# Kernel optimization log

Measured on AMD Instinct MI355X. Metric: run time of the kernel, lower is better.

Reference implementation:

```python
import jax, jax.numpy as jnp
import numpy as np

N, Z, E, M0, M1, D = 16384, 100, 400, 4000, 2000, 4


def setup_inputs() -> dict:
    key = jax.random.key(0)
    k = jax.random.split(key, 7)
    return {
        "theta": jax.random.normal(k[0], (N, Z), jnp.float32),
        "alpha0": jax.random.normal(k[1], (M0, E), jnp.float32),
        "alpha1": jax.random.normal(k[2], (M1, E), jnp.float32),
        "beta": jax.random.normal(k[3], (Z, E), jnp.float32),
        "bias0": jax.random.normal(k[4], (D, M0), jnp.float32),
        "bias1": jax.random.normal(k[5], (D, M1), jnp.float32),
        "domain_idx": jax.random.randint(k[6], (N,), 0, D, dtype=jnp.int32),
    }


def _recon_mod(theta, alpha, beta, bias, domain_idx):
    # Topic_mod = (alpha @ beta.T).T == beta @ alpha.T : (Z, M)
    topic = beta @ alpha.T
    # per-domain GEMM + indexed bias-add + log_softmax + scatter-back
    # == single GEMM with per-row gathered bias (all domains present)
    logits = theta @ topic + bias[domain_idx]  # (N, M)
    return jax.nn.log_softmax(logits, axis=-1)


def reference(theta, alpha0, alpha1, beta, bias0, bias1, domain_idx):
    r0 = _recon_mod(theta, alpha0, beta, bias0, domain_idx)
    r1 = _recon_mod(theta, alpha1, beta, bias1, domain_idx)
    return (r0, r1)
```

## Files before the change

### kernel.cpp

```cpp
#include <hip/hip_runtime.h>
#include <hip/hip_bf16.h>

#define PN 16384
#define PZ 100
#define PE 400
#define PM0 4000
#define PM1 2000
#define KP 128
#define SEG1ROW 4096
#define MROWS 6144

typedef __attribute__((ext_vector_type(8))) _Float16 half8v;
typedef __attribute__((ext_vector_type(4))) float floatx4;
typedef __attribute__((ext_vector_type(4))) unsigned int uint4v;

__global__ __launch_bounds__(256) void fill_kernel(uint4v* __restrict__ p, int n16)
{
    int i = blockIdx.x * 256 + threadIdx.x;
    if (i < n16) p[i] = (uint4v){0u, 0u, 0u, 0u};
}

__global__ __launch_bounds__(256) void topic_kernel(
    const float* __restrict__ alpha0, const float* __restrict__ alpha1,
    const float* __restrict__ beta, _Float16* __restrict__ b2t)
{
    const int seg = (blockIdx.x >= 64);
    const int tile = seg ? (blockIdx.x - 64) : blockIdx.x;
    const float* alpha = seg ? alpha1 : alpha0;
    const int M = seg ? PM1 : PM0;
    const int rowbase = seg ? SEG1ROW : 0;

    __shared__ float sA[64][201];
    const int tid = threadIdx.x;
    const int ml = tid & 63;
    const int zt = tid >> 6;
    const int m0 = tile * 64;
    const int z0 = blockIdx.y * 20 + zt * 5;

    float acc[5] = {0.f, 0.f, 0.f, 0.f, 0.f};

    for (int ec = 0; ec < 2; ++ec) {
        #pragma unroll
        for (int l = 0; l < 50; ++l) {
            int idx = tid + l * 256;
            int mr = idx / 200;
            int e  = idx - mr * 200;
            int m  = m0 + mr;
            sA[mr][e] = (m < M) ? alpha[(size_t)m * PE + ec * 200 + e] : 0.f;
        }
        __syncthreads();
        const float* bz = beta + (size_t)z0 * PE + ec * 200;
        #pragma unroll 4
        for (int e = 0; e < 200; ++e) {
            float a = sA[ml][e];
            #pragma unroll
            for (int zi = 0; zi < 5; ++zi)
                acc[zi] = fmaf(bz[zi * PE + e], a, acc[zi]);
        }
        __syncthreads();
    }
    int m = m0 + ml;
    if (m < M) {
        #pragma unroll
        for (int zi = 0; zi < 5; ++zi)
            b2t[(size_t)(rowbase + m) * KP + (z0 + zi)] = (_Float16)acc[zi];
    }
}

__global__ __launch_bounds__(512, 4) void fused_kernel(
    const float* __restrict__ theta,
    const _Float16* __restrict__ B2T,
    const float* __restrict__ bias0, const float* __restrict__ bias1,
    const int* __restrict__ dom,
    float* __restrict__ out0, float* __restrict__ out1)
{
    __shared__ __align__(1024) char sA[8192];
    __shared__ float smx[8][32];
    __shared__ float sms[8][32];
    __shared__ float slse[32];

    const int tid = threadIdx.x;
    const int w   = tid >> 6;
    const int ll  = tid & 63;
    const int g   = ll >> 4;
    const int c   = ll & 15;
    const int n0  = blockIdx.x * 32;

    {
        int row  = tid >> 4;
        int slot = tid & 15;
        const float* tr = theta + (size_t)(n0 + row) * PZ + slot * 8;
        half8v h;
        if (slot < 12) {
            float4 lo = *(const float4*)tr;
            float4 hi = *(const float4*)(tr + 4);
            h[0] = (_Float16)lo.x; h[1] = (_Float16)lo.y;
            h[2] = (_Float16)lo.z; h[3] = (_Float16)lo.w;
            h[4] = (_Float16)hi.x; h[5] = (_Float16)hi.y;
            h[6] = (_Float16)hi.z; h[7] = (_Float16)hi.w;
        } else if (slot == 12) {
            float4 lo = *(const float4*)tr;
            h[0] = (_Float16)lo.x; h[1] = (_Float16)lo.y;
            h[2] = (_Float16)lo.z; h[3] = (_Float16)lo.w;
            h[4] = (_Float16)0.f; h[5] = (_Float16)0.f;
            h[6] = (_Float16)0.f; h[7] = (_Float16)0.f;
        } else {
            h = (half8v)(_Float16)0.f;
        }
        *(half8v*)(sA + row * 256 + ((slot ^ (row & 7)) * 16)) = h;
    }
    __syncthreads();

    half8v aF[2][4];
    #pragma unroll
    for (int mi = 0; mi < 2; ++mi) {
        int row = mi * 16 + c;
        #pragma unroll
        for (int kb = 0; kb < 4; ++kb) {
            int slot = (kb * 4 + g) ^ (row & 7);
            aF[mi][kb] = *(const half8v*)(sA + row * 256 + slot * 16);
        }
    }

    int drow[2][4];
    #pragma unroll
    for (int mi = 0; mi < 2; ++mi)
        #pragma unroll
        for (int i = 0; i < 4; ++i)
            drow[mi][i] = dom[n0 + mi * 16 + 4 * g + i];

    for (int seg = 0; seg < 2; ++seg) {
        const int Mse = seg ? PM1 : PM0;
        const int NT  = seg ? 16 : 32;
        const _Float16* Bseg = B2T + (size_t)(seg ? SEG1ROW : 0) * KP;
        const float* bias = seg ? bias1 : bias0;
        float* out = seg ? out1 : out0;

        const _Float16* bcol = Bseg + (size_t)(w * 16 + c) * KP;
        const int mbase = w * 16 + c;

        float mx_[2][4], sm_[2][4];
        #pragma unroll
        for (int mi = 0; mi < 2; ++mi)
            #pragma unroll
            for (int i = 0; i < 4; ++i) { mx_[mi][i] = -3.0e38f; sm_[mi][i] = 0.f; }

        for (int t = 0; t < NT; ++t) {
            const int m  = t * 128 + mbase;
            const _Float16* bp = bcol + (size_t)t * 128 * KP;
            half8v bF[4];
            #pragma unroll
            for (int kb = 0; kb < 4; ++kb)
                bF[kb] = *(const half8v*)(bp + kb * 32 + g * 8);

            const bool mv = (m < Mse);
            const int mc = mv ? m : (Mse - 1);
            float bv0 = bias[mc];
            float bv1 = bias[(size_t)Mse + mc];
            float bv2 = bias[2 * (size_t)Mse + mc];
            float bv3 = bias[3 * (size_t)Mse + mc];

            floatx4 acc[2];
            acc[0] = (floatx4){0.f, 0.f, 0.f, 0.f};
            acc[1] = (floatx4){0.f, 0.f, 0.f, 0.f};
            #pragma unroll
            for (int mi = 0; mi < 2; ++mi)
                #pragma unroll
                for (int kb = 0; kb < 4; ++kb)
                    acc[mi] = __builtin_amdgcn_mfma_f32_16x16x32_f16(
                        aF[mi][kb], bF[kb], acc[mi], 0, 0, 0);

            float vv[2][4];
            float gm = -3.0e38f;
            #pragma unroll
            for (int mi = 0; mi < 2; ++mi) {
                #pragma unroll
                for (int i = 0; i < 4; ++i) {
                    int d = drow[mi][i];
                    float bv = (d < 2) ? (d == 0 ? bv0 : bv1) : (d == 2 ? bv2 : bv3);
                    float v = mv ? (acc[mi][i] + bv) : -1.0e30f;
                    vv[mi][i] = v;
                    gm = fmaxf(gm, v - mx_[mi][i]);
                }
            }
            if (gm <= 8.0f) {
                #pragma unroll
                for (int mi = 0; mi < 2; ++mi)
                    #pragma unroll
                    for (int i = 0; i < 4; ++i)
                        sm_[mi][i] += __expf(vv[mi][i] - mx_[mi][i]);
            } else {
                #pragma unroll
                for (int mi = 0; mi < 2; ++mi) {
                    #pragma unroll
                    for (int i = 0; i < 4; ++i) {
                        float v  = vv[mi][i];
                        float nm = fmaxf(mx_[mi][i], v);
                        sm_[mi][i] = sm_[mi][i] * __expf(mx_[mi][i] - nm)
                                   + __expf(v - nm);
                        mx_[mi][i] = nm;
                    }
                }
            }
        }

        #pragma unroll
        for (int mi = 0; mi < 2; ++mi) {
            #pragma unroll
            for (int i = 0; i < 4; ++i) {
                float m_ = mx_[mi][i], s_ = sm_[mi][i];
                #pragma unroll
                for (int msk = 1; msk < 16; msk <<= 1) {
                    float mo = __shfl_xor(m_, msk);
                    float so = __shfl_xor(s_, msk);
                    float nm = fmaxf(m_, mo);
                    s_ = s_ * __expf(m_ - nm) + so * __expf(mo - nm);
                    m_ = nm;
                }
                if (c == 0) {
                    int row = mi * 16 + 4 * g + i;
                    smx[w][row] = m_;
                    sms[w][row] = s_;
                }
            }
        }
        __syncthreads();
        if (tid < 32) {
            float m_ = smx[0][tid], s_ = sms[0][tid];
            #pragma unroll
            for (int wv = 1; wv < 8; ++wv) {
                float mo = smx[wv][tid];
                float so = sms[wv][tid];
                float nm = fmaxf(m_, mo);
                s_ = s_ * __expf(m_ - nm) + so * __expf(mo - nm);
                m_ = nm;
            }
            slse[tid] = m_ + __logf(s_);
        }
        __syncthreads();
        float lse_[2][4];
        #pragma unroll
        for (int mi = 0; mi < 2; ++mi)
            #pragma unroll
            for (int i = 0; i < 4; ++i)
                lse_[mi][i] = slse[mi * 16 + 4 * g + i];
        __syncthreads();

        for (int t = 0; t < NT; ++t) {
            const int m  = t * 128 + mbase;
            const _Float16* bp = bcol + (size_t)t * 128 * KP;
            half8v bF[4];
            #pragma unroll
            for (int kb = 0; kb < 4; ++kb)
                bF[kb] = *(const half8v*)(bp + kb * 32 + g * 8);

            const bool mv = (m < Mse);
            const int mc = mv ? m : (Mse - 1);
            float bv0 = bias[mc];
            float bv1 = bias[(size_t)Mse + mc];
            float bv2 = bias[2 * (size_t)Mse + mc];
            float bv3 = bias[3 * (size_t)Mse + mc];

            floatx4 acc[2];
            acc[0] = (floatx4){0.f, 0.f, 0.f, 0.f};
            acc[1] = (floatx4){0.f, 0.f, 0.f, 0.f};
            #pragma unroll
            for (int mi = 0; mi < 2; ++mi)
                #pragma unroll
                for (int kb = 0; kb < 4; ++kb)
                    acc[mi] = __builtin_amdgcn_mfma_f32_16x16x32_f16(
                        aF[mi][kb], bF[kb], acc[mi], 0, 0, 0);

            if (mv) {
                #pragma unroll
                for (int mi = 0; mi < 2; ++mi) {
                    #pragma unroll
                    for (int i = 0; i < 4; ++i) {
                        int row = mi * 16 + 4 * g + i;
                        int d = drow[mi][i];
                        float bv = (d < 2) ? (d == 0 ? bv0 : bv1)
                                           : (d == 2 ? bv2 : bv3);
                        float o = acc[mi][i] + bv - lse_[mi][i];
                        __builtin_nontemporal_store(
                            o, &out[(size_t)(n0 + row) * Mse + m]);
                    }
                }
            }
        }
    }
}

extern "C" void kernel_launch(void* const* d_in, const int* in_sizes, int n_in,
                              void* d_out, int out_size, void* d_ws, size_t ws_size,
                              hipStream_t stream) {
    const float* theta  = (const float*)d_in[0];
    const float* alpha0 = (const float*)d_in[1];
    const float* alpha1 = (const float*)d_in[2];
    const float* beta   = (const float*)d_in[3];
    const float* bias0  = (const float*)d_in[4];
    const float* bias1  = (const float*)d_in[5];
    const int*   dom    = (const int*)d_in[6];

    float* out0 = (float*)d_out;
    float* out1 = out0 + (size_t)PN * PM0;

    _Float16* B2T = (_Float16*)d_ws;

    {
        int n16 = MROWS * KP * 2 / 16;
        fill_kernel<<<(n16 + 255) / 256, 256, 0, stream>>>((uint4v*)B2T, n16);
    }

    topic_kernel<<<dim3(96, 5), 256, 0, stream>>>(alpha0, alpha1, beta, B2T);

    fused_kernel<<<PN / 32, 512, 0, stream>>>(
        theta, B2T, bias0, bias1, dom, out0, out1);
}
```

Before: 315.1 us.

## Fold per-domain bias into GEMM via one-hot K columns; prefetch B tiles

Each theta row gets a one-hot domain vector in the padded K columns (100..103), and the topic kernel writes the matching bias rows into B2T, so the MFMA now produces logits with the bias already added. This removes the four scalar bias gathers and the per-element domain select from both passes of the fused kernel. The topic kernel now computes all 100 topics per block, stages its output in LDS and zeroes the padding itself, which drops the separate fill kernel launch. The fused kernel double-buffers B fragment loads across tiles. The risk is that bias is now rounded to fp16 inside the GEMM, which changes precision, and the topic kernel runs on far fewer blocks with more registers each.

```diff
diff --git a/kernel.cpp b/kernel.cpp
--- a/kernel.cpp
+++ b/kernel.cpp
@@ -14,30 +14,33 @@
 typedef __attribute__((ext_vector_type(4))) float floatx4;
 typedef __attribute__((ext_vector_type(4))) unsigned int uint4v;
 
-__global__ __launch_bounds__(256) void fill_kernel(uint4v* __restrict__ p, int n16)
-{
-    int i = blockIdx.x * 256 + threadIdx.x;
-    if (i < n16) p[i] = (uint4v){0u, 0u, 0u, 0u};
-}
-
 __global__ __launch_bounds__(256) void topic_kernel(
     const float* __restrict__ alpha0, const float* __restrict__ alpha1,
-    const float* __restrict__ beta, _Float16* __restrict__ b2t)
+    const float* __restrict__ beta,
+    const float* __restrict__ bias0, const float* __restrict__ bias1,
+    _Float16* __restrict__ b2t)
 {
+    __shared__ __align__(16) char lds[64 * 201 * 4];
+    float* sAl = (float*)lds;
+    _Float16* st = (_Float16*)lds;
+
     const int seg = (blockIdx.x >= 64);
-    const int tile = seg ? (blockIdx.x - 64) : blockIdx.x;
+    const int bt  = seg ? (blockIdx.x - 64) : blockIdx.x;
     const float* alpha = seg ? alpha1 : alpha0;
-    const int M = seg ? PM1 : PM0;
-    const int rowbase = seg ? SEG1ROW : 0;
-
-    __shared__ float sA[64][201];
+    const float* bias  = seg ? bias1 : bias0;
+    const int Mse = seg ? PM1 : PM0;
+    const int rowbase = (seg ? SEG1ROW : 0) + bt * 64;
+    const int m0 = bt * 64;
+
     const int tid = threadIdx.x;
     const int ml = tid & 63;
     const int zt = tid >> 6;
-    const int m0 = tile * 64;
-    const int z0 = blockIdx.y * 20 + zt * 5;
-
-    float acc[5] = {0.f, 0.f, 0.f, 0.f, 0.f};
+    const int m  = m0 + ml;
+    const bool mvalid = (m < Mse);
+
+    float acc[25];
+    #pragma unroll
+    for (int j = 0; j < 25; ++j) acc[j] = 0.f;
 
     for (int ec = 0; ec < 2; ++ec) {
         #pragma unroll
@@ -45,36 +48,50 @@
             int idx = tid + l * 256;
             int mr = idx / 200;
             int e  = idx - mr * 200;
-            int m  = m0 + mr;
-            sA[mr][e] = (m < M) ? alpha[(size_t)m * PE + ec * 200 + e] : 0.f;
-        }
-        __syncthreads();
-        const float* bz = beta + (size_t)z0 * PE + ec * 200;
-        #pragma unroll 4
+            int mm = m0 + mr;
+            sAl[mr * 201 + e] = (mm < Mse) ? alpha[(size_t)mm * PE + ec * 200 + e] : 0.f;
+        }
+        __syncthreads();
+        const float* bz = beta + (size_t)(zt * 25) * PE + ec * 200;
         for (int e = 0; e < 200; ++e) {
-            float a = sA[ml][e];
-            #pragma unroll
-            for (int zi = 0; zi < 5; ++zi)
-                acc[zi] = fmaf(bz[zi * PE + e], a, acc[zi]);
-        }
-        __syncthreads();
-    }
-    int m = m0 + ml;
-    if (m < M) {
-        #pragma unroll
-        for (int zi = 0; zi < 5; ++zi)
-            b2t[(size_t)(rowbase + m) * KP + (z0 + zi)] = (_Float16)acc[zi];
+            float a = sAl[ml * 201 + e];
+            #pragma unroll
+            for (int j = 0; j < 25; ++j)
+                acc[j] = fmaf(bz[(size_t)j * PE + e], a, acc[j]);
+        }
+        __syncthreads();
+    }
+
+    #pragma unroll
+    for (int j = 0; j < 25; ++j)
+        st[ml * 128 + zt * 25 + j] = mvalid ? (_Float16)acc[j] : (_Float16)0.f;
+    {
+        int mr = tid >> 2, d = tid & 3;
+        int mm = m0 + mr;
+        st[mr * 128 + 100 + d] =
+            (mm < Mse) ? (_Float16)bias[(size_t)d * Mse + mm] : (_Float16)0.f;
+    }
+    for (int idx = tid; idx < 64 * 24; idx += 256) {
+        int r = idx / 24, k = 104 + idx - (idx / 24) * 24;
+        st[r * 128 + k] = (_Float16)0.f;
+    }
+    __syncthreads();
+
+    #pragma unroll
+    for (int it = 0; it < 4; ++it) {
+        int off = it * 4096 + tid * 16;
+        uint4v v = *(const uint4v*)((const char*)st + off);
+        *(uint4v*)((char*)b2t + (size_t)rowbase * 256 + off) = v;
     }
 }
 
 __global__ __launch_bounds__(512, 4) void fused_kernel(
     const float* __restrict__ theta,
     const _Float16* __restrict__ B2T,
-    const float* __restrict__ bias0, const float* __restrict__ bias1,
     const int* __restrict__ dom,
     float* __restrict__ out0, float* __restrict__ out1)
 {
-    __shared__ __align__(1024) char sA[8192];
+    __shared__ __align__(1024) char sA[32 * 256];
     __shared__ float smx[8][32];
     __shared__ float sms[8][32];
     __shared__ float slse[32];
@@ -90,7 +107,7 @@
         int row  = tid >> 4;
         int slot = tid & 15;
         const float* tr = theta + (size_t)(n0 + row) * PZ + slot * 8;
-        half8v h;
+        half8v h = (half8v)(_Float16)0.f;
         if (slot < 12) {
             float4 lo = *(const float4*)tr;
             float4 hi = *(const float4*)(tr + 4);
@@ -102,10 +119,11 @@
             float4 lo = *(const float4*)tr;
             h[0] = (_Float16)lo.x; h[1] = (_Float16)lo.y;
             h[2] = (_Float16)lo.z; h[3] = (_Float16)lo.w;
-            h[4] = (_Float16)0.f; h[5] = (_Float16)0.f;
-            h[6] = (_Float16)0.f; h[7] = (_Float16)0.f;
-        } else {
-            h = (half8v)(_Float16)0.f;
+            int d = dom[n0 + row];
+            h[4] = (_Float16)(d == 0 ? 1.f : 0.f);
+            h[5] = (_Float16)(d == 1 ? 1.f : 0.f);
+            h[6] = (_Float16)(d == 2 ? 1.f : 0.f);
+            h[7] = (_Float16)(d == 3 ? 1.f : 0.f);
         }
         *(half8v*)(sA + row * 256 + ((slot ^ (row & 7)) * 16)) = h;
     }
@@ -122,22 +140,16 @@
         }
     }
 
-    int drow[2][4];
-    #pragma unroll
-    for (int mi = 0; mi < 2; ++mi)
-        #pragma unroll
-        for (int i = 0; i < 4; ++i)
-            drow[mi][i] = dom[n0 + mi * 16 + 4 * g + i];
+    const int mbase = w * 16 + c;
 
     for (int seg = 0; seg < 2; ++seg) {
         const int Mse = seg ? PM1 : PM0;
         const int NT  = seg ? 16 : 32;
         const _Float16* Bseg = B2T + (size_t)(seg ? SEG1ROW : 0) * KP;
-        const float* bias = seg ? bias1 : bias0;
         float* out = seg ? out1 : out0;
 
-        const _Float16* bcol = Bseg + (size_t)(w * 16 + c) * KP;
-        const int mbase = w * 16 + c;
+        const _Float16* bp0 = Bseg + (size_t)mbase * KP;
+        const size_t TSTEP = (size_t)128 * KP;
 
         float mx_[2][4], sm_[2][4];
         #pragma unroll
@@ -145,44 +157,32 @@
             #pragma unroll
             for (int i = 0; i < 4; ++i) { mx_[mi][i] = -3.0e38f; sm_[mi][i] = 0.f; }
 
-        for (int t = 0; t < NT; ++t) {
-            const int m  = t * 128 + mbase;
-            const _Float16* bp = bcol + (size_t)t * 128 * KP;
-            half8v bF[4];
+        auto loadB = [&](half8v (&bf)[4], const _Float16* p) {
             #pragma unroll
             for (int kb = 0; kb < 4; ++kb)
-                bF[kb] = *(const half8v*)(bp + kb * 32 + g * 8);
-
-            const bool mv = (m < Mse);
-            const int mc = mv ? m : (Mse - 1);
-            float bv0 = bias[mc];
-            float bv1 = bias[(size_t)Mse + mc];
-            float bv2 = bias[2 * (size_t)Mse + mc];
-            float bv3 = bias[3 * (size_t)Mse + mc];
-
-            floatx4 acc[2];
-            acc[0] = (floatx4){0.f, 0.f, 0.f, 0.f};
-            acc[1] = (floatx4){0.f, 0.f, 0.f, 0.f};
-            #pragma unroll
-            for (int mi = 0; mi < 2; ++mi)
-                #pragma unroll
-                for (int kb = 0; kb < 4; ++kb)
-                    acc[mi] = __builtin_amdgcn_mfma_f32_16x16x32_f16(
-                        aF[mi][kb], bF[kb], acc[mi], 0, 0, 0);
-
+                bf[kb] = *(const half8v*)(p + kb * 32 + g * 8);
+        };
+        auto mfma8 = [&](half8v (&bf)[4], floatx4& a0, floatx4& a1) {
+            a0 = (floatx4){0.f, 0.f, 0.f, 0.f};
+            a1 = (floatx4){0.f, 0.f, 0.f, 0.f};
+            #pragma unroll
+            for (int kb = 0; kb < 4; ++kb) {
+                a0 = __builtin_amdgcn_mfma_f32_16x16x32_f16(aF[0][kb], bf[kb], a0, 0, 0, 0);
+                a1 = __builtin_amdgcn_mfma_f32_16x16x32_f16(aF[1][kb], bf[kb], a1, 0, 0, 0);
+            }
+        };
+        auto stats_step = [&](floatx4& a0, floatx4& a1, int t) {
+            const bool mv = (t * 128 + mbase) < Mse;
             float vv[2][4];
             float gm = -3.0e38f;
             #pragma unroll
-            for (int mi = 0; mi < 2; ++mi) {
+            for (int mi = 0; mi < 2; ++mi)
                 #pragma unroll
                 for (int i = 0; i < 4; ++i) {
-                    int d = drow[mi][i];
-                    float bv = (d < 2) ? (d == 0 ? bv0 : bv1) : (d == 2 ? bv2 : bv3);
-                    float v = mv ? (acc[mi][i] + bv) : -1.0e30f;
+                    float v = mv ? (mi ? a1[i] : a0[i]) : -1.0e30f;
                     vv[mi][i] = v;
                     gm = fmaxf(gm, v - mx_[mi][i]);
                 }
-            }
             if (gm <= 8.0f) {
                 #pragma unroll
                 for (int mi = 0; mi < 2; ++mi)
@@ -191,16 +191,30 @@
                         sm_[mi][i] += __expf(vv[mi][i] - mx_[mi][i]);
             } else {
                 #pragma unroll
-                for (int mi = 0; mi < 2; ++mi) {
+                for (int mi = 0; mi < 2; ++mi)
                     #pragma unroll
                     for (int i = 0; i < 4; ++i) {
                         float v  = vv[mi][i];
                         float nm = fmaxf(mx_[mi][i], v);
-                        sm_[mi][i] = sm_[mi][i] * __expf(mx_[mi][i] - nm)
-                                   + __expf(v - nm);
+                        sm_[mi][i] = sm_[mi][i] * __expf(mx_[mi][i] - nm) + __expf(v - nm);
                         mx_[mi][i] = nm;
                     }
-                }
+            }
+        };
+
+        {
+            half8v bA[4], bB[4];
+            floatx4 a0, a1;
+            const _Float16* bp = bp0;
+            loadB(bA, bp);
+            for (int t = 0; t < NT; t += 2) {
+                loadB(bB, bp + TSTEP);
+                mfma8(bA, a0, a1);
+                stats_step(a0, a1, t);
+                if (t + 2 < NT) loadB(bA, bp + 2 * TSTEP);
+                mfma8(bB, a0, a1);
+                stats_step(a0, a1, t + 1);
+                bp += 2 * TSTEP;
             }
         }
 
@@ -246,45 +260,44 @@
                 lse_[mi][i] = slse[mi * 16 + 4 * g + i];
         __syncthreads();
 
-        for (int t = 0; t < NT; ++t) {
-            const int m  = t * 128 + mbase;
-            const _Float16* bp = bcol + (size_t)t * 128 * KP;
-            half8v bF[4];
-            #pragma unroll
-            for (int kb = 0; kb < 4; ++kb)
-                bF[kb] = *(const half8v*)(bp + kb * 32 + g * 8);
-
-            const bool mv = (m < Mse);
-            const int mc = mv ? m : (Mse - 1);
-            float bv0 = bias[mc];
-            float bv1 = bias[(size_t)Mse + mc];
-            float bv2 = bias[2 * (size_t)Mse + mc];
-            float bv3 = bias[3 * (size_t)Mse + mc];
-
-            floatx4 acc[2];
-            acc[0] = (floatx4){0.f, 0.f, 0.f, 0.f};
-            acc[1] = (floatx4){0.f, 0.f, 0.f, 0.f};
+        {
+            float* op[2][4];
             #pragma unroll
             for (int mi = 0; mi < 2; ++mi)
                 #pragma unroll
-                for (int kb = 0; kb < 4; ++kb)
-                    acc[mi] = __builtin_amdgcn_mfma_f32_16x16x32_f16(
-                        aF[mi][kb], bF[kb], acc[mi], 0, 0, 0);
-
-            if (mv) {
-                #pragma unroll
-                for (int mi = 0; mi < 2; ++mi) {
+                for (int i = 0; i < 4; ++i)
+                    op[mi][i] = out + (size_t)(n0 + mi * 16 + 4 * g + i) * Mse + mbase;
+
+            auto write_step = [&](floatx4& a0, floatx4& a1, int t) {
+                const bool mv = (t * 128 + mbase) < Mse;
+                if (mv) {
                     #pragma unroll
-                    for (int i = 0; i < 4; ++i) {
-                        int row = mi * 16 + 4 * g + i;
-                        int d = drow[mi][i];
-                        float bv = (d < 2) ? (d == 0 ? bv0 : bv1)
-                                           : (d == 2 ? bv2 : bv3);
-                        float o = acc[mi][i] + bv - lse_[mi][i];
-                        __builtin_nontemporal_store(
-                            o, &out[(size_t)(n0 + row) * Mse + m]);
-                    }
+                    for (int mi = 0; mi < 2; ++mi)
+                        #pragma unroll
+                        for (int i = 0; i < 4; ++i) {
+                            float o = (mi ? a1[i] : a0[i]) - lse_[mi][i];
+                            __builtin_nontemporal_store(o, op[mi][i]);
+                        }
                 }
+                #pragma unroll
+                for (int mi = 0; mi < 2; ++mi)
+                    #pragma unroll
+                    for (int i = 0; i < 4; ++i)
+                        op[mi][i] += 128;
+            };
+
+            half8v bA[4], bB[4];
+            floatx4 a0, a1;
+            const _Float16* bp = bp0;
+            loadB(bA, bp);
+            for (int t = 0; t < NT; t += 2) {
+                loadB(bB, bp + TSTEP);
+                mfma8(bA, a0, a1);
+                write_step(a0, a1, t);
+                if (t + 2 < NT) loadB(bA, bp + 2 * TSTEP);
+                mfma8(bB, a0, a1);
+                write_step(a0, a1, t + 1);
+                bp += 2 * TSTEP;
             }
         }
     }
@@ -306,13 +319,7 @@
 
     _Float16* B2T = (_Float16*)d_ws;
 
-    {
-        int n16 = MROWS * KP * 2 / 16;
-        fill_kernel<<<(n16 + 255) / 256, 256, 0, stream>>>((uint4v*)B2T, n16);
-    }
-
-    topic_kernel<<<dim3(96, 5), 256, 0, stream>>>(alpha0, alpha1, beta, B2T);
-
-    fused_kernel<<<PN / 32, 512, 0, stream>>>(
-        theta, B2T, bias0, bias1, dom, out0, out1);
+    topic_kernel<<<96, 256, 0, stream>>>(alpha0, alpha1, beta, bias0, bias1, B2T);
+
+    fused_kernel<<<PN / 32, 512, 0, stream>>>(theta, B2T, dom, out0, out1);
 }
```

New measurement: 425.0 us. 34.9% more time.
